# Performance work log

Hardware: AMD Instinct MI355X
Metric: run time of the kernel (lower is better)

Reference implementation:

```python
import jax, jax.numpy as jnp
import numpy as np

B, N, C = 32, 1000, 81
MAX_INST = 100
MIN_CONF = 0.7
NMS_THRESH = 0.3
WINDOW = (0.0, 0.0, 1.0, 1.0)  # normalized y1, x1, y2, x2


def _apply_deltas(boxes, deltas):
    # boxes, deltas: [N, 4] in (y1, x1, y2, x2) / (dy, dx, log_dh, log_dw)
    h = boxes[:, 2] - boxes[:, 0]
    w = boxes[:, 3] - boxes[:, 1]
    cy = boxes[:, 0] + 0.5 * h + deltas[:, 0] * h
    cx = boxes[:, 1] + 0.5 * w + deltas[:, 1] * w
    h = h * jnp.exp(deltas[:, 2])
    w = w * jnp.exp(deltas[:, 3])
    y1 = cy - 0.5 * h
    x1 = cx - 0.5 * w
    return jnp.stack([y1, x1, y1 + h, x1 + w], axis=1)


def _clip_boxes(boxes, window):
    wy1, wx1, wy2, wx2 = window
    return jnp.stack([
        jnp.clip(boxes[:, 0], wy1, wy2),
        jnp.clip(boxes[:, 1], wx1, wx2),
        jnp.clip(boxes[:, 2], wy1, wy2),
        jnp.clip(boxes[:, 3], wx1, wx2)], axis=1)


def _pairwise_iou(b):
    y1, x1, y2, x2 = b[:, 0], b[:, 1], b[:, 2], b[:, 3]
    area = (y2 - y1) * (x2 - x1)
    iy = jnp.maximum(jnp.minimum(y2[:, None], y2[None, :]) - jnp.maximum(y1[:, None], y1[None, :]), 0.0)
    ix = jnp.maximum(jnp.minimum(x2[:, None], x2[None, :]) - jnp.maximum(x1[:, None], x1[None, :]), 0.0)
    inter = iy * ix
    union = area[:, None] + area[None, :] - inter
    return inter / jnp.maximum(union, 1e-8)


def _refine_one(rois, probs, deltas, std_dev):
    n = rois.shape[0]
    class_ids = jnp.argmax(probs, axis=1)                 # [N]
    scores = jnp.max(probs, axis=1)                       # [N]
    # per-roi deltas for the predicted class, scaled by bbox_std_dev
    d = jnp.take_along_axis(deltas, class_ids[:, None, None], axis=1)[:, 0, :] * std_dev
    boxes = _clip_boxes(_apply_deltas(rois, d), WINDOW)   # [N, 4]
    valid = (class_ids > 0) & (scores >= MIN_CONF)        # drop background + low conf

    # sort by score descending (invalid at the end)
    order = jnp.argsort(-jnp.where(valid, scores, -jnp.inf))
    b = boxes[order]
    s = scores[order]
    c = class_ids[order]
    v = valid[order]

    # greedy per-class NMS on score-sorted boxes
    iou = _pairwise_iou(b)                                # [N, N]
    sup = (iou > NMS_THRESH) & (c[:, None] == c[None, :])
    idx = jnp.arange(n)

    def step(keep, i):
        row = sup[i] & (idx > i) & keep[i]
        return keep & ~row, None

    keep, _ = jax.lax.scan(step, v, jnp.arange(n))
    keep = jax.lax.stop_gradient(keep)

    # kept boxes are already score-ordered -> compact first MAX_INST into slots
    slot = jnp.where(keep, jnp.cumsum(keep) - 1, MAX_INST)
    slot = jnp.minimum(slot, MAX_INST)                    # overflow bucket
    rows = jnp.concatenate([b, c[:, None].astype(b.dtype), s[:, None]], axis=1)  # [N, 6]
    out = jnp.zeros((MAX_INST + 1, 6), b.dtype).at[slot].set(rows)[:MAX_INST]
    return out                                            # [MAX_INST, 6]


def setup_inputs() -> dict:
    key = jax.random.key(0)
    k1, k2, k3, k4, k5 = jax.random.split(key, 5)
    cy = jax.random.uniform(k1, (B, N))
    cx = jax.random.uniform(k2, (B, N))
    h = jax.random.uniform(k3, (B, N), minval=0.02, maxval=0.4)
    w = jax.random.uniform(k4, (B, N), minval=0.02, maxval=0.4)
    rois = jnp.stack([
        jnp.clip(cy - 0.5 * h, 0.0, 1.0),
        jnp.clip(cx - 0.5 * w, 0.0, 1.0),
        jnp.clip(cy + 0.5 * h, 0.0, 1.0),
        jnp.clip(cx + 0.5 * w, 0.0, 1.0)], axis=2).astype(jnp.float32)
    logits = jax.random.normal(k5, (B, N, C), dtype=jnp.float32) * 2.0
    mrcnn_class = jax.nn.softmax(logits, axis=-1)
    mrcnn_bbox = jax.random.normal(jax.random.fold_in(key, 7), (B, N, C, 4), dtype=jnp.float32)
    bbox_std_dev = jnp.array([0.1, 0.1, 0.2, 0.2], dtype=jnp.float32)
    return {"rois": rois, "mrcnn_class": mrcnn_class, "mrcnn_bbox": mrcnn_bbox, "bbox_std_dev": bbox_std_dev}


def reference(rois, mrcnn_class, mrcnn_bbox, bbox_std_dev):
    out = jax.vmap(lambda r, p, d: _refine_one(r, p, d, bbox_std_dev))(rois, mrcnn_class, mrcnn_bbox)
    return out.reshape(B, MAX_INST, 6)
```

## Files before the change

### kernel.cpp

```cpp
#include <hip/hip_runtime.h>
#include <math.h>

#define BB 32
#define NN 1000
#define CC 81
#define MAX_INST 100
#define MIN_CONF 0.7f
#define NMS_THRESH 0.3f
#define MCAP 1024
#define RCHUNK 192
#define WMAX 16


__global__ __launch_bounds__(256) void roi_kernel(
    const float* __restrict__ rois,
    const float* __restrict__ probs,
    const float* __restrict__ deltas,
    const float* __restrict__ std_dev,
    int* __restrict__ gcnt,
    float* __restrict__ glist,
    float* __restrict__ out)
{
  if (blockIdx.x == 0) {
    float4* o4 = (float4*)out;
    for (int i = threadIdx.x; i < BB * MAX_INST * 6 / 4; i += 256)
      o4[i] = make_float4(0.f, 0.f, 0.f, 0.f);
  }

  int wg = blockIdx.x * 4 + (threadIdx.x >> 6);
  if (wg >= BB * NN) return;
  int lane = threadIdx.x & 63;

  const float* p = probs + (size_t)wg * CC;
  float v = p[lane];
  int   c = lane;
  if (lane + 64 < CC) {
    float v2 = p[lane + 64];
    if (v2 > v) { v = v2; c = lane + 64; }
  }
  for (int off = 32; off; off >>= 1) {
    float vo = __shfl_down(v, off);
    int   co = __shfl_down(c, off);
    if (vo > v || (vo == v && co < c)) { v = vo; c = co; }
  }

  if (lane == 0 && c > 0 && v >= MIN_CONF) {
    float4 dd = *(const float4*)(deltas + ((size_t)wg * CC + c) * 4);
    float4 r4 = *(const float4*)(rois + (size_t)wg * 4);
    float dy = dd.x * std_dev[0], dx = dd.y * std_dev[1];
    float dh = dd.z * std_dev[2], dw = dd.w * std_dev[3];
    float h = r4.z - r4.x, w = r4.w - r4.y;
    float cy = r4.x + 0.5f * h + dy * h;
    float cx = r4.y + 0.5f * w + dx * w;
    h *= expf(dh); w *= expf(dw);
    float y1 = cy - 0.5f * h, x1 = cx - 0.5f * w;
    float y2 = y1 + h,        x2 = x1 + w;
    y1 = fminf(fmaxf(y1, 0.f), 1.f); x1 = fminf(fmaxf(x1, 0.f), 1.f);
    y2 = fminf(fmaxf(y2, 0.f), 1.f); x2 = fminf(fmaxf(x2, 0.f), 1.f);
    int b = wg / NN, n = wg - b * NN;
    int pos = atomicAdd(&gcnt[b], 1);
    float4* o = (float4*)(glist + ((size_t)b * MCAP + pos) * 8);
    o[0] = make_float4(y1, x1, y2, x2);
    o[1] = make_float4(v, (float)c, (float)n, 0.f);
  }
}

__global__ __launch_bounds__(256) void nms_kernel(
    const int* __restrict__ gcnt,
    const float* __restrict__ glist,
    float* __restrict__ out)
{
  const int b = blockIdx.x, t = threadIdx.x;

  __shared__ float cscore[MCAP];
  __shared__ int   cidx[MCAP];
  __shared__ float sy1[MCAP], sx1[MCAP], sy2[MCAP], sx2[MCAP];
  __shared__ int   scls[MCAP];
  __shared__ float sscr[MCAP];
  __shared__ unsigned long long rows[RCHUNK][WMAX];
  __shared__ unsigned long long keepw[WMAX];

  const int M = gcnt[b];
  const int W = (M + 63) >> 6;
  const float* base = glist + (size_t)b * MCAP * 8;

  for (int e = t; e < M; e += 256) {
    const float4 s = ((const float4*)(base + (size_t)e * 8))[1];
    cscore[e] = s.x; cidx[e] = (int)s.z;
  }
  __syncthreads();

  for (int e = t; e < M; e += 256) {
    const float4 a = ((const float4*)(base + (size_t)e * 8))[0];
    const float4 s = ((const float4*)(base + (size_t)e * 8))[1];
    float sc = s.x; int oi = (int)s.z;
    int r = 0;
    for (int j = 0; j < M; ++j) {
      float sj = cscore[j]; int ij = cidx[j];
      if (sj > sc || (sj == sc && ij < oi)) ++r;
    }
    sy1[r] = a.x; sx1[r] = a.y; sy2[r] = a.z; sx2[r] = a.w;
    scls[r] = (int)s.y; sscr[r] = sc;
  }
  if (t < WMAX) {
    unsigned long long kw = 0ULL;
    int nb = M - t * 64;
    if (nb > 0) kw = (nb >= 64) ? ~0ULL : ((1ULL << nb) - 1ULL);
    keepw[t] = kw;
  }
  __syncthreads();

  const int wv = t >> 6, lane = t & 63;
  for (int c0 = 0; c0 < M; c0 += RCHUNK) {
    int R = min(RCHUNK, M - c0);
    for (int task = wv; task < R * W; task += 4) {
      int i = c0 + task / W;
      int w = task % W;
      int j = w * 64 + lane;
      bool cond = false;
      float iy1 = sy1[i], ix1 = sx1[i], iy2 = sy2[i], ix2 = sx2[i];
      int ic = scls[i];
      if (j < M && j > i && scls[j] == ic) {
        float jy1 = sy1[j], jx1 = sx1[j], jy2 = sy2[j], jx2 = sx2[j];
        float ai = (iy2 - iy1) * (ix2 - ix1);
        float aj = (jy2 - jy1) * (jx2 - jx1);
        float iy = fmaxf(fminf(iy2, jy2) - fmaxf(iy1, jy1), 0.f);
        float ix = fmaxf(fminf(ix2, jx2) - fmaxf(ix1, jx1), 0.f);
        float inter = iy * ix;
        float uni = fmaxf(ai + aj - inter, 1e-8f);
        cond = (inter / uni) > NMS_THRESH;
      }
      unsigned long long word = __ballot(cond);
      if (lane == 0) rows[task / W][w] = word;
    }
    __syncthreads();
    if (t < 64) {
      unsigned long long kw = (t < W) ? keepw[t] : 0ULL;
      for (int i = c0; i < c0 + R; ++i) {
        unsigned long long kwi = __shfl((long long)kw, i >> 6);
        if ((kwi >> (i & 63)) & 1ULL) {
          if (t < W) kw &= ~rows[i - c0][t];
        }
      }
      if (t < W) keepw[t] = kw;
    }
    __syncthreads();
  }

  for (int r = t; r < M; r += 256) {
    unsigned long long kwme = keepw[r >> 6];
    if ((kwme >> (r & 63)) & 1ULL) {
      int slot = 0;
      for (int w = 0; w < (r >> 6); ++w) slot += __popcll(keepw[w]);
      slot += __popcll(kwme & ((1ULL << (r & 63)) - 1ULL));
      if (slot < MAX_INST) {
        float* o = out + ((size_t)b * MAX_INST + slot) * 6;
        o[0] = sy1[r]; o[1] = sx1[r]; o[2] = sy2[r]; o[3] = sx2[r];
        o[4] = (float)scls[r]; o[5] = sscr[r];
      }
    }
  }
}

extern "C" void kernel_launch(void* const* d_in, const int* in_sizes, int n_in,
                              void* d_out, int out_size, void* d_ws, size_t ws_size,
                              hipStream_t stream) {
  const float* rois    = (const float*)d_in[0];
  const float* probs   = (const float*)d_in[1];
  const float* deltas  = (const float*)d_in[2];
  const float* std_dev = (const float*)d_in[3];
  float* out = (float*)d_out;

  int*   gcnt  = (int*)d_ws;
  float* glist = (float*)((char*)d_ws + 128);

  hipMemsetAsync(gcnt, 0, 128, stream);
  roi_kernel<<<(BB * NN + 3) / 4, 256, 0, stream>>>(rois, probs, deltas, std_dev,
                                                    gcnt, glist, out);
  nms_kernel<<<BB, 256, 0, stream>>>(gcnt, glist, out);
}
```

Baseline: 104.8 us.

## Fuse memset, ROI refinement and NMS into one cooperative kernel with grid sync

Replaces the memset plus two kernel launches with a single cooperative kernel of 512 blocks that zeroes counters and output, runs the per-ROI argmax and box refinement in a grid-stride loop, grid-syncs, and then runs NMS on the first 32 blocks. The aim is to cut launch overhead and inter-kernel gaps. RCHUNK also drops from 192 to 128, which reduces shared memory so more blocks can be co-resident. In exchange it pays for two grid-wide barriers, requires every block to be resident at once, and adds an extra threadfence.

```diff
diff --git a/kernel.cpp b/kernel.cpp
--- a/kernel.cpp
+++ b/kernel.cpp
@@ -1,5 +1,8 @@
 #include <hip/hip_runtime.h>
+#include <hip/hip_cooperative_groups.h>
 #include <math.h>
+
+namespace cg = cooperative_groups;
 
 #define BB 32
 #define NN 1000
@@ -8,11 +11,13 @@
 #define MIN_CONF 0.7f
 #define NMS_THRESH 0.3f
 #define MCAP 1024
-#define RCHUNK 192
+#define RCHUNK 128
 #define WMAX 16
+#define NBLK 512
+#define NTHR 256
 
 
-__global__ __launch_bounds__(256) void roi_kernel(
+__global__ __launch_bounds__(NTHR) void fused_detection_kernel(
     const float* __restrict__ rois,
     const float* __restrict__ probs,
     const float* __restrict__ deltas,
@@ -21,56 +26,10 @@
     float* __restrict__ glist,
     float* __restrict__ out)
 {
-  if (blockIdx.x == 0) {
-    float4* o4 = (float4*)out;
-    for (int i = threadIdx.x; i < BB * MAX_INST * 6 / 4; i += 256)
-      o4[i] = make_float4(0.f, 0.f, 0.f, 0.f);
-  }
-
-  int wg = blockIdx.x * 4 + (threadIdx.x >> 6);
-  if (wg >= BB * NN) return;
-  int lane = threadIdx.x & 63;
-
-  const float* p = probs + (size_t)wg * CC;
-  float v = p[lane];
-  int   c = lane;
-  if (lane + 64 < CC) {
-    float v2 = p[lane + 64];
-    if (v2 > v) { v = v2; c = lane + 64; }
-  }
-  for (int off = 32; off; off >>= 1) {
-    float vo = __shfl_down(v, off);
-    int   co = __shfl_down(c, off);
-    if (vo > v || (vo == v && co < c)) { v = vo; c = co; }
-  }
-
-  if (lane == 0 && c > 0 && v >= MIN_CONF) {
-    float4 dd = *(const float4*)(deltas + ((size_t)wg * CC + c) * 4);
-    float4 r4 = *(const float4*)(rois + (size_t)wg * 4);
-    float dy = dd.x * std_dev[0], dx = dd.y * std_dev[1];
-    float dh = dd.z * std_dev[2], dw = dd.w * std_dev[3];
-    float h = r4.z - r4.x, w = r4.w - r4.y;
-    float cy = r4.x + 0.5f * h + dy * h;
-    float cx = r4.y + 0.5f * w + dx * w;
-    h *= expf(dh); w *= expf(dw);
-    float y1 = cy - 0.5f * h, x1 = cx - 0.5f * w;
-    float y2 = y1 + h,        x2 = x1 + w;
-    y1 = fminf(fmaxf(y1, 0.f), 1.f); x1 = fminf(fmaxf(x1, 0.f), 1.f);
-    y2 = fminf(fmaxf(y2, 0.f), 1.f); x2 = fminf(fmaxf(x2, 0.f), 1.f);
-    int b = wg / NN, n = wg - b * NN;
-    int pos = atomicAdd(&gcnt[b], 1);
-    float4* o = (float4*)(glist + ((size_t)b * MCAP + pos) * 8);
-    o[0] = make_float4(y1, x1, y2, x2);
-    o[1] = make_float4(v, (float)c, (float)n, 0.f);
-  }
-}
-
-__global__ __launch_bounds__(256) void nms_kernel(
-    const int* __restrict__ gcnt,
-    const float* __restrict__ glist,
-    float* __restrict__ out)
-{
-  const int b = blockIdx.x, t = threadIdx.x;
+  cg::grid_group grid = cg::this_grid();
+  const int t    = threadIdx.x;
+  const int blk  = blockIdx.x;
+  const int gtid = blk * NTHR + t;
 
   __shared__ float cscore[MCAP];
   __shared__ int   cidx[MCAP];
@@ -80,17 +39,65 @@
   __shared__ unsigned long long rows[RCHUNK][WMAX];
   __shared__ unsigned long long keepw[WMAX];
 
+  if (gtid < BB) gcnt[gtid] = 0;
+  {
+    float4* o4 = (float4*)out;
+    const int n4 = BB * MAX_INST * 6 / 4;
+    if (gtid < n4) o4[gtid] = make_float4(0.f, 0.f, 0.f, 0.f);
+  }
+  grid.sync();
+
+  const int lane  = t & 63;
+  const int gwave = gtid >> 6;
+  for (int wg = gwave; wg < BB * NN; wg += (NBLK * NTHR) / 64) {
+    const float* p = probs + (size_t)wg * CC;
+    float v = p[lane];
+    int   c = lane;
+    if (lane + 64 < CC) {
+      float v2 = p[lane + 64];
+      if (v2 > v) { v = v2; c = lane + 64; }
+    }
+    for (int off = 32; off; off >>= 1) {
+      float vo = __shfl_down(v, off);
+      int   co = __shfl_down(c, off);
+      if (vo > v || (vo == v && co < c)) { v = vo; c = co; }
+    }
+    if (lane == 0 && c > 0 && v >= MIN_CONF) {
+      float4 dd = *(const float4*)(deltas + ((size_t)wg * CC + c) * 4);
+      float4 r4 = *(const float4*)(rois + (size_t)wg * 4);
+      float dy = dd.x * std_dev[0], dx = dd.y * std_dev[1];
+      float dh = dd.z * std_dev[2], dw = dd.w * std_dev[3];
+      float h = r4.z - r4.x, w = r4.w - r4.y;
+      float cy = r4.x + 0.5f * h + dy * h;
+      float cx = r4.y + 0.5f * w + dx * w;
+      h *= expf(dh); w *= expf(dw);
+      float y1 = cy - 0.5f * h, x1 = cx - 0.5f * w;
+      float y2 = y1 + h,        x2 = x1 + w;
+      y1 = fminf(fmaxf(y1, 0.f), 1.f); x1 = fminf(fmaxf(x1, 0.f), 1.f);
+      y2 = fminf(fmaxf(y2, 0.f), 1.f); x2 = fminf(fmaxf(x2, 0.f), 1.f);
+      int b = wg / NN, n = wg - b * NN;
+      int pos = atomicAdd(&gcnt[b], 1);
+      float4* o = (float4*)(glist + ((size_t)b * MCAP + pos) * 8);
+      o[0] = make_float4(y1, x1, y2, x2);
+      o[1] = make_float4(v, (float)c, (float)n, 0.f);
+    }
+  }
+  __threadfence();
+  grid.sync();
+
+  if (blk >= BB) return;
+  const int b = blk;
   const int M = gcnt[b];
   const int W = (M + 63) >> 6;
   const float* base = glist + (size_t)b * MCAP * 8;
 
-  for (int e = t; e < M; e += 256) {
+  for (int e = t; e < M; e += NTHR) {
     const float4 s = ((const float4*)(base + (size_t)e * 8))[1];
     cscore[e] = s.x; cidx[e] = (int)s.z;
   }
   __syncthreads();
 
-  for (int e = t; e < M; e += 256) {
+  for (int e = t; e < M; e += NTHR) {
     const float4 a = ((const float4*)(base + (size_t)e * 8))[0];
     const float4 s = ((const float4*)(base + (size_t)e * 8))[1];
     float sc = s.x; int oi = (int)s.z;
@@ -110,7 +117,7 @@
   }
   __syncthreads();
 
-  const int wv = t >> 6, lane = t & 63;
+  const int wv = t >> 6;
   for (int c0 = 0; c0 < M; c0 += RCHUNK) {
     int R = min(RCHUNK, M - c0);
     for (int task = wv; task < R * W; task += 4) {
@@ -147,7 +154,7 @@
     __syncthreads();
   }
 
-  for (int r = t; r < M; r += 256) {
+  for (int r = t; r < M; r += NTHR) {
     unsigned long long kwme = keepw[r >> 6];
     if ((kwme >> (r & 63)) & 1ULL) {
       int slot = 0;
@@ -172,10 +179,10 @@
   float* out = (float*)d_out;
 
   int*   gcnt  = (int*)d_ws;
-  float* glist = (float*)((char*)d_ws + 128);
+  float* glist = (float*)((char*)d_ws + 256);
 
-  hipMemsetAsync(gcnt, 0, 128, stream);
-  roi_kernel<<<(BB * NN + 3) / 4, 256, 0, stream>>>(rois, probs, deltas, std_dev,
-                                                    gcnt, glist, out);
-  nms_kernel<<<BB, 256, 0, stream>>>(gcnt, glist, out);
+  void* args[] = { (void*)&rois, (void*)&probs, (void*)&deltas, (void*)&std_dev,
+                   (void*)&gcnt, (void*)&glist, (void*)&out };
+  hipLaunchCooperativeKernel((const void*)fused_detection_kernel,
+                             dim3(NBLK), dim3(NTHR), args, 0, stream);
 }
```

Result: slower. 248.4 us (+136.9%).
